# Optimization experiments

Measured on AMD Instinct MI355X. Metric: run time of the kernel, lower is better.

Reference implementation:

```python
import math
import jax, jax.numpy as jnp
import numpy as np

B, L, E, H, NL = 8, 512, 512, 8, 2


def setup_inputs() -> dict:
    key = jax.random.key(0)
    ks = jax.random.split(key, 12)
    s = 0.02  # weight init scale
    return {
        "inputs_4e": jax.random.normal(ks[0], (B, L, 4 * E), jnp.float32),
        "query_embed": jax.random.normal(ks[1], (B, L, E), jnp.float32),
        "rel": jax.random.normal(ks[2], (B, L, L), jnp.float32),
        "resp_rel": jax.random.normal(ks[3], (B, L, L), jnp.float32),
        "timestamp": jax.random.uniform(ks[4], (B, L, L), jnp.float32) * 10.0,
        "l1": jax.random.uniform(ks[5], (1,), jnp.float32),
        "l2": jax.random.uniform(ks[6], (1,), jnp.float32),
        "l3": jax.random.uniform(ks[7], (1,), jnp.float32),
        "Win": jax.random.normal(ks[8], (4 * E, E), jnp.float32) * s,
        "b_in": jnp.zeros((E,), jnp.float32),
        "Wqkv": jax.random.normal(ks[9], (NL, 3, E, E), jnp.float32) * s,
        "bqkv": jnp.zeros((NL, 3, E), jnp.float32),
        "Wf1": jax.random.normal(ks[10], (2 * E, E), jnp.float32) * s,
        "bf1": jnp.zeros((E,), jnp.float32),
        "Wf2": jax.random.normal(ks[11], (E, 1), jnp.float32) * s,
        "bf2": jnp.zeros((1,), jnp.float32),
    }


def _mha(q_in, k_in, v_in, Wq, bq, Wk, bk, Wv, bv,
         rel, resp_rel, timestamp, l1, l2, l3, mask):
    Bb, Ll, Ee = q_in.shape
    d = Ee // H

    def split(x, W, b):  # (B,L,E) -> (B,H,L,d)
        return (x @ W + b).reshape(Bb, Ll, H, d).transpose(0, 2, 1, 3)

    q = split(q_in, Wq, bq)
    k = split(k_in, Wk, bk)
    v = split(v_in, Wv, bv)

    # relation softmax: zero out where mask==False, -1e4 at zeros
    maskf = mask.astype(rel.dtype)              # (1,1,L,L)
    rel_m = rel[:, None, :, :] * maskf          # (B,1,L,L), broadcasts over heads
    rel_attn = jax.nn.softmax(jnp.where(rel_m == 0, -1e4, rel_m), axis=-1)
    resp_m = resp_rel[:, None, :, :] * maskf
    resp_attn = jax.nn.softmax(jnp.where(resp_m == 0, -1e4, resp_m), axis=-1)

    # QK softmax with causal mask
    scores = jnp.einsum('bhqd,bhkd->bhqk', q, k) / math.sqrt(d)
    scores = jnp.where(mask, -1e9, scores)
    prob_attn = jax.nn.softmax(scores, axis=-1)

    # time-decay softmax
    ts = jnp.exp(-jnp.abs(timestamp))[:, None, :, :]  # (B,1,L,L)
    ts = jnp.where(mask, -jnp.inf, ts)
    time_attn = jax.nn.softmax(ts, axis=-1)

    # blend (ablation flags all True)
    p = (1.0 - l2) * prob_attn + l2 * time_attn
    p = (1.0 - l1) * p + l1 * rel_attn
    p = (1.0 - l3) * p + l3 * resp_attn

    out = jnp.einsum('bhqk,bhkd->bhqd', p, v)
    out = out.transpose(0, 2, 1, 3).reshape(Bb, Ll, Ee)
    return out, p


def reference(inputs_4e, query_embed, rel, resp_rel, timestamp,
              l1, l2, l3, Win, b_in, Wqkv, bqkv, Wf1, bf1, Wf2, bf2):
    mask = jnp.triu(jnp.ones((1, 1, L, L), dtype=bool), k=1)  # future mask
    inputs = jax.nn.relu(inputs_4e @ Win + b_in)              # lin_in_interaction

    outputs, attn = _mha(query_embed, inputs, inputs,
                         Wqkv[0, 0], bqkv[0, 0], Wqkv[0, 1], bqkv[0, 1],
                         Wqkv[0, 2], bqkv[0, 2],
                         rel, resp_rel, timestamp, l1, l2, l3, mask)
    for i in range(1, NL):
        residual, attn = _mha(query_embed, outputs, outputs,
                              Wqkv[i, 0], bqkv[i, 0], Wqkv[i, 1], bqkv[i, 1],
                              Wqkv[i, 2], bqkv[i, 2],
                              rel, resp_rel, timestamp, l1, l2, l3, mask)
        outputs = outputs + jax.nn.relu(residual)

    concat_q = jnp.concatenate([outputs, query_embed], axis=-1)  # (B,L,2E)
    h = jax.nn.relu(concat_q @ Wf1 + bf1)
    return h @ Wf2 + bf2  # (B,L,1)
```

## Files before the change

kernel.cpp:

```cpp
#include <hip/hip_runtime.h>
#include <math.h>

namespace {
constexpr int B = 8, L = 512, E = 512, H = 8;
constexpr int M = B * L;
}

typedef float f32x4 __attribute__((ext_vector_type(4)));
typedef short bf16x8 __attribute__((ext_vector_type(8)));

__device__ inline ushort f2b(float f) {
  unsigned u = __float_as_uint(f);
  u += 0x7FFF + ((u >> 16) & 1);
  return (ushort)(u >> 16);
}
__device__ inline float b2f(ushort h) { return __uint_as_float(((unsigned)h) << 16); }

__device__ inline f32x4 mfma16(bf16x8 a, bf16x8 b, f32x4 c) {
  return __builtin_amdgcn_mfma_f32_16x16x32_bf16(a, b, c, 0, 0, 0);
}

__device__ __forceinline__ void gl2lds16(const ushort* g, ushort* l) {
  __builtin_amdgcn_global_load_lds(
      (const __attribute__((address_space(1))) void*)g,
      (__attribute__((address_space(3))) void*)l, 16, 0, 0);
}

template <int NROWS>
__device__ __forceinline__ void stage64(const ushort* __restrict__ g, int ldg,
                                        ushort* lds, int tid) {
  const int w = tid >> 6, l = tid & 63;
  constexpr int RPW = NROWS / 4;
  constexpr int NI = RPW / 8;
#pragma unroll
  for (int it = 0; it < NI; ++it) {
    const int rbase = w * RPW + it * 8;
    const int row = rbase + (l >> 3);
    const int chunk = (l & 7) ^ (row & 7);
    gl2lds16(g + (size_t)row * ldg + chunk * 8, lds + rbase * 64);
  }
}

template <int BM, int NBUF>
__device__ __forceinline__ void stage_comb(const ushort* b0, const ushort* b1,
                                           const ushort* b2, const ushort* b3,
                                           ushort* lds, int tid) {
#pragma unroll
  for (int it = 0; it < BM / 32; ++it) {
    const int row = (tid >> 3) + it * 32;
    const int slot = tid & 7;
    const size_t off = (size_t)row * 512 + slot * 8;
    union Uu { uint4 u; ushort s[8]; } va, vb, vc, vd, vo;
    va.u = *(const uint4*)(b0 + off);
    vb.u = *(const uint4*)(b1 + off);
    if (NBUF == 4) {
      vc.u = *(const uint4*)(b2 + off);
      vd.u = *(const uint4*)(b3 + off);
    }
#pragma unroll
    for (int e = 0; e < 8; ++e) {
      float f = b2f(va.s[e]) + b2f(vb.s[e]);
      if (NBUF == 4) f += fmaxf(b2f(vc.s[e]) + b2f(vd.s[e]), 0.f);
      vo.s[e] = f2b(f);
    }
    *(uint4*)(&lds[row * 64 + ((slot ^ (row & 7)) * 8)]) = vo.u;
  }
}

template <int BM, int MODE, int HAS_BIAS, int ACT, int STAGEA, int FUSE>
__device__ __forceinline__ void dev_gemm(
    ushort* lds, int bxx, int by, const ushort* A, const ushort* A2,
    const ushort* A3, const ushort* A4, const ushort* Aq,
    const ushort* Wt, const float* bias, ushort* C0, ushort* C1, ushort* C2,
    const float* w2, float* outv, int K, int N) {
  ushort* Als = lds;
  ushort* Bls = lds + 2 * BM * 64;
  const int tid = threadIdx.x;
  const int l = tid & 63, wv = tid >> 6;
  const int wr = wv >> 1, wc = wv & 1;
  const int g = l >> 4, c = l & 15;
  constexpr int WM = BM / 2;
  constexpr int MFR = WM / 16;
  const int bm = by * BM;
  const int bn64 = bxx * 64;
  const int sec = (MODE == 5) ? (bn64 >> 9) : 0;
  const bool vsec = (MODE == 5 && sec == 1);

  const ushort* Ause = (MODE == 5) ? A2 : A;
  const int ldA = K;
  const ushort* Bp = Wt + (size_t)bn64 * K;

  f32x4 acc[MFR][2];
#pragma unroll
  for (int mi = 0; mi < MFR; ++mi)
#pragma unroll
    for (int ni = 0; ni < 2; ++ni) acc[mi][ni] = f32x4{0.f, 0.f, 0.f, 0.f};

  auto stageA = [&](int t, int buf) {
    ushort* dst = Als + buf * BM * 64;
    if (STAGEA == 0) {
      stage64<BM>(Ause + (size_t)bm * ldA + t * 64, ldA, dst, tid);
    } else if (STAGEA == 2) {
      stage_comb<BM, 2>(A + (size_t)bm * 512 + t * 64,
                        A2 + (size_t)bm * 512 + t * 64, nullptr, nullptr, dst, tid);
    } else {
      if (t < 8)
        stage_comb<BM, 4>(A + (size_t)bm * 512 + t * 64,
                          A2 + (size_t)bm * 512 + t * 64,
                          A3 + (size_t)bm * 512 + t * 64,
                          A4 + (size_t)bm * 512 + t * 64, dst, tid);
      else
        stage64<BM>(Aq + (size_t)bm * 512 + (t - 8) * 64, 512, dst, tid);
    }
  };

  stageA(0, 0);
  stage64<64>(Bp, K, Bls, tid);
  __syncthreads();

  const int NT = K >> 6;
  int cur = 0;
  for (int t = 0; t < NT; ++t) {
    if (t + 1 < NT) {
      stageA(t + 1, cur ^ 1);
      stage64<64>(Bp + (t + 1) * 64, K, Bls + (cur ^ 1) * 64 * 64, tid);
    }
#pragma unroll
    for (int ks = 0; ks < 2; ++ks) {
      bf16x8 af[MFR], bf_[2];
#pragma unroll
      for (int mi = 0; mi < MFR; ++mi) {
        const int row = wr * WM + mi * 16 + c;
        af[mi] = *(const bf16x8*)(&Als[cur * BM * 64 + row * 64 +
                                       (((ks * 4 + g) ^ (row & 7)) * 8)]);
      }
#pragma unroll
      for (int ni = 0; ni < 2; ++ni) {
        const int row = wc * 32 + ni * 16 + c;
        bf_[ni] = *(const bf16x8*)(&Bls[cur * 64 * 64 + row * 64 +
                                        (((ks * 4 + g) ^ (row & 7)) * 8)]);
      }
      if (vsec) {
#pragma unroll
        for (int mi = 0; mi < MFR; ++mi)
#pragma unroll
          for (int ni = 0; ni < 2; ++ni)
            acc[mi][ni] = mfma16(bf_[ni], af[mi], acc[mi][ni]);
      } else {
#pragma unroll
        for (int mi = 0; mi < MFR; ++mi)
#pragma unroll
          for (int ni = 0; ni < 2; ++ni)
            acc[mi][ni] = mfma16(af[mi], bf_[ni], acc[mi][ni]);
      }
    }
    __syncthreads();
    cur ^= 1;
  }

  if (FUSE) {
    float w2v[2];
#pragma unroll
    for (int ni = 0; ni < 2; ++ni) w2v[ni] = w2[bn64 + wc * 32 + ni * 16 + c];
#pragma unroll
    for (int mi = 0; mi < MFR; ++mi) {
#pragma unroll
      for (int r = 0; r < 4; ++r) {
        float p = 0.f;
#pragma unroll
        for (int ni = 0; ni < 2; ++ni) {
          const int n = bn64 + wc * 32 + ni * 16 + c;
          float v = acc[mi][ni][r] + bias[n];
          v = fmaxf(v, 0.f);
          p += v * w2v[ni];
        }
        p += __shfl_xor(p, 1);
        p += __shfl_xor(p, 2);
        p += __shfl_xor(p, 4);
        p += __shfl_xor(p, 8);
        if (c == 0) atomicAdd(&outv[bm + wr * WM + mi * 16 + g * 4 + r], p);
      }
    }
  } else if (vsec) {
    const int e0 = bn64 - 512;
#pragma unroll
    for (int ni = 0; ni < 2; ++ni) {
#pragma unroll
      for (int r = 0; r < 4; ++r) {
        const int e = e0 + wc * 32 + ni * 16 + g * 4 + r;
        const float bv = HAS_BIAS ? bias[512 + e] : 0.f;
#pragma unroll
        for (int mi = 0; mi < MFR; ++mi) {
          const int m = bm + wr * WM + mi * 16 + c;
          const int bb = m >> 9, lt = m & 511;
          C2[((size_t)bb * 512 + e) * 512 + lt] = f2b(acc[mi][ni][r] + bv);
        }
      }
    }
  } else {
    ushort* dst = (MODE == 5) ? C1 : C0;
    const int nsub = (MODE == 5) ? sec * 512 : 0;
    const int ldc = (MODE == 5) ? 512 : N;
#pragma unroll
    for (int ni = 0; ni < 2; ++ni) {
      const int n = bn64 + wc * 32 + ni * 16 + c;
      const float bv = HAS_BIAS ? bias[n] : 0.f;
#pragma unroll
      for (int mi = 0; mi < MFR; ++mi) {
#pragma unroll
        for (int r = 0; r < 4; ++r) {
          const int m = bm + wr * WM + mi * 16 + g * 4 + r;
          float v = acc[mi][ni][r] + bv;
          if (ACT) v = fmaxf(v, 0.f);
          dst[(size_t)m * ldc + (n - nsub)] = f2b(v);
        }
      }
    }
  }
}

__device__ __forceinline__ void dev_attn(ushort* lds, int qt, int h, int b,
                                         const ushort* __restrict__ Qg,
                                         const ushort* __restrict__ Kg,
                                         const ushort* __restrict__ Vt,
                                         float c_p, ushort* __restrict__ aexp) {
  ushort* Qs = lds;
  ushort* Ps = lds + 4096;
  ushort* Ks = lds + 8192;
  ushort* Vs = lds + 16384;
  const int tid = threadIdx.x, l = tid & 63, w = tid >> 6;
  const int g = l >> 4, c = l & 15;
  const int qrow0 = b * L + qt * 64;
  const ushort* Kbase = Kg + (size_t)(b * L) * E + h * 64;
  const ushort* Vbase = Vt + (size_t)(b * E + h * 64) * L;

  stage64<64>(Qg + (size_t)qrow0 * E + h * 64, E, Qs, tid);
  stage64<64>(Kbase, E, Ks, tid);
  stage64<64>(Vbase, L, Vs, tid);
  __syncthreads();

  f32x4 o[4];
#pragma unroll
  for (int dn = 0; dn < 4; ++dn) o[dn] = f32x4{0.f, 0.f, 0.f, 0.f};
  float l_r[4] = {0.f, 0.f, 0.f, 0.f};

  int cur = 0;
  for (int kt = 0; kt <= qt; ++kt) {
    if (kt < qt) {
      stage64<64>(Kbase + (size_t)(kt + 1) * 64 * E, E, Ks + (cur ^ 1) * 4096, tid);
      stage64<64>(Vbase + (kt + 1) * 64, L, Vs + (cur ^ 1) * 4096, tid);
    }
    bf16x8 qf[2];
#pragma unroll
    for (int kq = 0; kq < 2; ++kq) {
      int row = w * 16 + c;
      qf[kq] = *(const bf16x8*)(&Qs[row * 64 + (((kq * 4 + g) ^ (row & 7)) * 8)]);
    }
    f32x4 s4[4];
#pragma unroll
    for (int n = 0; n < 4; ++n) s4[n] = f32x4{0.f, 0.f, 0.f, 0.f};
#pragma unroll
    for (int n = 0; n < 4; ++n) {
#pragma unroll
      for (int kq = 0; kq < 2; ++kq) {
        int row = n * 16 + c;
        bf16x8 kf = *(const bf16x8*)(&Ks[cur * 4096 + row * 64 +
                                         (((kq * 4 + g) ^ (row & 7)) * 8)]);
        s4[n] = mfma16(qf[kq], kf, s4[n]);
      }
    }
    const bool diag = (kt == qt);
    float pv[4][4];
    float lad[4] = {0.f, 0.f, 0.f, 0.f};
#pragma unroll
    for (int n = 0; n < 4; ++n)
#pragma unroll
      for (int r = 0; r < 4; ++r) {
        float sv = s4[n][r] * 0.125f;
        if (diag && (n * 16 + c) > (w * 16 + g * 4 + r)) sv = -1e30f;
        float p = __expf(sv);
        pv[n][r] = p;
        lad[r] += p;
      }
#pragma unroll
    for (int off = 1; off < 16; off <<= 1)
#pragma unroll
      for (int r = 0; r < 4; ++r) lad[r] += __shfl_xor(lad[r], off);
#pragma unroll
    for (int r = 0; r < 4; ++r) l_r[r] += lad[r];
#pragma unroll
    for (int n = 0; n < 4; ++n)
#pragma unroll
      for (int r = 0; r < 4; ++r) {
        int q = w * 16 + g * 4 + r;
        int byt = 32 * n + 2 * c;
        int slot = byt >> 4;
        Ps[q * 64 + ((slot ^ (q & 7)) * 8) + ((byt & 15) >> 1)] = f2b(pv[n][r]);
      }
    bf16x8 pf[2];
#pragma unroll
    for (int kq = 0; kq < 2; ++kq) {
      int row = w * 16 + c;
      pf[kq] = *(const bf16x8*)(&Ps[row * 64 + (((kq * 4 + g) ^ (row & 7)) * 8)]);
    }
#pragma unroll
    for (int dn = 0; dn < 4; ++dn) {
#pragma unroll
      for (int kq = 0; kq < 2; ++kq) {
        int row = dn * 16 + c;
        bf16x8 vf = *(const bf16x8*)(&Vs[cur * 4096 + row * 64 +
                                         (((kq * 4 + g) ^ (row & 7)) * 8)]);
        o[dn] = mfma16(pf[kq], vf, o[dn]);
      }
    }
    __syncthreads();
    cur ^= 1;
  }

  float linv[4];
#pragma unroll
  for (int r = 0; r < 4; ++r) linv[r] = c_p / l_r[r];
#pragma unroll
  for (int dn = 0; dn < 4; ++dn) {
#pragma unroll
    for (int r = 0; r < 4; ++r) {
      const size_t row = (size_t)qrow0 + w * 16 + g * 4 + r;
      const int col = h * 64 + dn * 16 + c;
      aexp[row * E + col] = f2b(o[dn][r] * linv[r]);
    }
  }
}

__device__ __forceinline__ void dev_blend(int idx, const float* __restrict__ rel,
                                          const float* __restrict__ resp,
                                          const float* __restrict__ ts,
                                          float l1, float l2, float l3,
                                          ushort* __restrict__ stat) {
  const float c_t = (1.f - l3) * (1.f - l1) * l2;
  const float c_r = (1.f - l3) * l1;
  const float c_s = l3;
  const int wave = threadIdx.x >> 6, lane = threadIdx.x & 63;
  const int row = idx * 4 + wave;
  const int qi = row & (L - 1);
  const size_t base = (size_t)row * L;
  float rv[8], sv[8], tv[8];
#pragma unroll
  for (int jj = 0; jj < 8; ++jj) {
    const int k = jj * 64 + lane;
    const float r = rel[base + k];
    const float s = resp[base + k];
    const float tt = ts[base + k];
    const bool fut = (k > qi);
    const float rm = fut ? r : 0.f;
    const float sm = fut ? s : 0.f;
    rv[jj] = (rm == 0.f) ? -1e4f : rm;
    sv[jj] = (sm == 0.f) ? -1e4f : sm;
    tv[jj] = fut ? -INFINITY : __expf(-fabsf(tt));
  }
  float rmax = -INFINITY, smax = -INFINITY, tmax = -INFINITY;
#pragma unroll
  for (int jj = 0; jj < 8; ++jj) {
    rmax = fmaxf(rmax, rv[jj]); smax = fmaxf(smax, sv[jj]); tmax = fmaxf(tmax, tv[jj]);
  }
  for (int off = 1; off < 64; off <<= 1) {
    rmax = fmaxf(rmax, __shfl_xor(rmax, off));
    smax = fmaxf(smax, __shfl_xor(smax, off));
    tmax = fmaxf(tmax, __shfl_xor(tmax, off));
  }
  float rsum = 0.f, ssum = 0.f, tsum = 0.f;
#pragma unroll
  for (int jj = 0; jj < 8; ++jj) {
    rsum += __expf(rv[jj] - rmax); ssum += __expf(sv[jj] - smax); tsum += __expf(tv[jj] - tmax);
  }
  for (int off = 1; off < 64; off <<= 1) {
    rsum += __shfl_xor(rsum, off);
    ssum += __shfl_xor(ssum, off);
    tsum += __shfl_xor(tsum, off);
  }
  const float rinv = c_r / rsum, sinv = c_s / ssum, tinv = c_t / tsum;
#pragma unroll
  for (int jj = 0; jj < 8; ++jj) {
    stat[base + jj * 64 + lane] =
        f2b(__expf(rv[jj] - rmax) * rinv + __expf(sv[jj] - smax) * sinv +
            __expf(tv[jj] - tmax) * tinv);
  }
}

__device__ __forceinline__ void tcvt_body(const float* __restrict__ src,
                                          ushort* __restrict__ dst, int Kd, int Nd,
                                          int kb, int nb, int t, ushort (*T)[33]) {
  const int r = t >> 3, c4 = (t & 7) * 4;
  float4 v = *(const float4*)(src + (size_t)(kb + r) * Nd + nb + c4);
  T[r][c4 + 0] = f2b(v.x); T[r][c4 + 1] = f2b(v.y);
  T[r][c4 + 2] = f2b(v.z); T[r][c4 + 3] = f2b(v.w);
  __syncthreads();
  ushort4 ov = {T[c4 + 0][r], T[c4 + 1][r], T[c4 + 2][r], T[c4 + 3][r]};
  *(ushort4*)(&dst[(size_t)(nb + r) * Kd + kb + c4]) = ov;
}

__global__ __launch_bounds__(256) void k_prep(
    const float* __restrict__ x4e, const float* __restrict__ query,
    const float* __restrict__ Win, const float* __restrict__ Wqkv,
    const float* __restrict__ bf2, ushort* __restrict__ x4e_bf,
    ushort* __restrict__ qbf, ushort* __restrict__ Wint,
    ushort* __restrict__ Wqkvt, float* __restrict__ outv) {
  __shared__ ushort T[32][33];
  const int bi = blockIdx.x;
  const int t = threadIdx.x;
  const long long EE = (long long)E * E;
  if (bi < 2560) {
    const int N1 = M * 2048 / 4;
#pragma unroll
    for (int it = 0; it < 4; ++it) {
      int i = bi * 1024 + it * 256 + t;
      if (i < N1) {
        float4 v = ((const float4*)x4e)[i];
        ushort4 o = {f2b(v.x), f2b(v.y), f2b(v.z), f2b(v.w)};
        ((ushort4*)x4e_bf)[i] = o;
      } else {
        int j = i - N1;
        float4 v = ((const float4*)query)[j];
        ushort4 o = {f2b(v.x), f2b(v.y), f2b(v.z), f2b(v.w)};
        ((ushort4*)qbf)[j] = o;
      }
    }
    return;
  }
  if (bi < 3584) {
    const int idx = bi - 2560;
    tcvt_body(Win, Wint, 2048, 512, (idx >> 4) * 32, (idx & 15) * 32, t, T);
    return;
  }
  if (bi < 4096) {
    const int idx = bi - 3584;
    const int z = (idx >= 256) ? 3 : 0;
    const int r = idx & 255;
    tcvt_body(Wqkv + z * EE, Wqkvt + z * EE, 512, 512, (r >> 4) * 32,
              (r & 15) * 32, t, T);
    return;
  }
  {
    const int i = (bi - 4096) * 256 + t;
    const float b2 = bf2[0];
    float4 v = {b2, b2, b2, b2};
    ((float4*)outv)[i] = v;
  }
}

__global__ __launch_bounds__(256) void k_xgemm_blend(
    const ushort* __restrict__ x4e_bf, const ushort* __restrict__ query_bf,
    const ushort* __restrict__ Wint, const ushort* __restrict__ Wqkvt,
    const float* __restrict__ b_in, const float* __restrict__ bqkv,
    ushort* __restrict__ x_bf, ushort* __restrict__ q_bf,
    ushort* __restrict__ q1_bf, const float* __restrict__ Wqkv,
    const float* __restrict__ Wf1, ushort* __restrict__ Wqkvt_out,
    ushort* __restrict__ Wf1t, const float* __restrict__ rel,
    const float* __restrict__ resp, const float* __restrict__ ts,
    const float* __restrict__ l1p, const float* __restrict__ l2p,
    const float* __restrict__ l3p, ushort* __restrict__ stat) {
  extern __shared__ ushort lds[];
  const int bx = blockIdx.x;
  const long long EE = (long long)E * E;
  if (bx < 256) {
    dev_gemm<128, 1, 1, 1, 0, 0>(lds, bx >> 5, bx & 31, x4e_bf, nullptr, nullptr,
                                 nullptr, nullptr, Wint, b_in, x_bf, nullptr,
                                 nullptr, nullptr, nullptr, 2048, 512);
  } else if (bx < 512) {
    const int r = bx - 256;
    dev_gemm<128, 1, 1, 0, 0, 0>(lds, r >> 5, r & 31, query_bf, nullptr, nullptr,
                                 nullptr, nullptr, Wqkvt, bqkv, q_bf, nullptr,
                                 nullptr, nullptr, nullptr, 512, 512);
  } else if (bx < 768) {
    const int r = bx - 512;
    dev_gemm<128, 1, 1, 0, 0, 0>(lds, r >> 5, r & 31, query_bf, nullptr, nullptr,
                                 nullptr, nullptr, Wqkvt + 3 * EE, bqkv + 3 * E,
                                 q1_bf, nullptr, nullptr, nullptr, nullptr, 512, 512);
  } else if (bx < 1792) {
    const int idx = bx - 768;
    const int zmap[4] = {1, 2, 4, 5};
    const int z = zmap[idx >> 8];
    const int r = idx & 255;
    tcvt_body(Wqkv + z * EE, Wqkvt_out + z * EE, 512, 512, (r >> 4) * 32,
              (r & 15) * 32, threadIdx.x, (ushort(*)[33])lds);
  } else if (bx < 2304) {
    const int q = bx - 1792;
    tcvt_body(Wf1, Wf1t, 1024, 512, (q >> 4) * 32, (q & 15) * 32,
              threadIdx.x, (ushort(*)[33])lds);
  } else {
    dev_blend(bx - 2304, rel, resp, ts, l1p[0], l2p[0], l3p[0], stat);
  }
}

__global__ __launch_bounds__(256) void k_kv0(
    const ushort* __restrict__ x_bf, const ushort* __restrict__ Wt,
    const float* __restrict__ bias, ushort* __restrict__ k_bf,
    ushort* __restrict__ vt) {
  extern __shared__ ushort lds[];
  const int bx = blockIdx.x;
  dev_gemm<128, 5, 1, 0, 0, 0>(lds, bx >> 5, bx & 31, nullptr, x_bf,
                               nullptr, nullptr, nullptr, Wt, bias, nullptr,
                               k_bf, vt, nullptr, nullptr, 512, 1024);
}

__global__ __launch_bounds__(256) void k_attn_stat(
    const ushort* __restrict__ Qg, const ushort* __restrict__ Kg,
    const ushort* __restrict__ Vt, const ushort* __restrict__ stat,
    const float* __restrict__ l1p, const float* __restrict__ l2p,
    const float* __restrict__ l3p, ushort* __restrict__ aexp,
    ushort* __restrict__ ostat) {
  extern __shared__ ushort lds[];
  const int bx = blockIdx.x;
  if (bx < 512) {
    const int hb = bx & 63;
    const int qt = 7 - (bx >> 6);
    const int h = hb & 7, b = hb >> 3;
    const float l1 = l1p[0], l2 = l2p[0], l3 = l3p[0];
    const float c_p = (1.f - l3) * (1.f - l1) * (1.f - l2);
    dev_attn(lds, qt, h, b, Qg, Kg, Vt, c_p, aexp);
  } else {
    const int idx = bx - 512;
    const int n = idx >> 5;
    const int rem = idx & 31;
    const int bz = rem >> 2, m = rem & 3;
    const long long LLs = (long long)L * L, ELs = (long long)E * L;
    dev_gemm<128, 1, 0, 0, 0, 0>(lds, n, m, stat + bz * LLs, nullptr,
                                 nullptr, nullptr, nullptr, Vt + bz * ELs,
                                 nullptr, ostat + bz * ELs, nullptr, nullptr,
                                 nullptr, nullptr, 512, 512);
  }
}

__global__ __launch_bounds__(256) void k_kv1(
    const ushort* __restrict__ aexp0, const ushort* __restrict__ ostat0,
    const ushort* __restrict__ Wt, const float* __restrict__ bias,
    ushort* __restrict__ k_bf, ushort* __restrict__ vt) {
  extern __shared__ ushort lds[];
  const int bx = blockIdx.x;
  dev_gemm<128, 5, 1, 0, 2, 0>(lds, bx >> 5, bx & 31, aexp0, ostat0,
                               nullptr, nullptr, nullptr, Wt, bias, nullptr,
                               k_bf, vt, nullptr, nullptr, 512, 1024);
}

__global__ __launch_bounds__(256) void k_f1(
    const ushort* __restrict__ aexp0, const ushort* __restrict__ ostat0,
    const ushort* __restrict__ aexp1, const ushort* __restrict__ ostat1,
    const ushort* __restrict__ query_bf, const ushort* __restrict__ Wf1t,
    const float* __restrict__ bf1, const float* __restrict__ Wf2,
    float* __restrict__ outv) {
  extern __shared__ ushort lds[];
  const int bx = blockIdx.x;
  dev_gemm<128, 4, 1, 1, 4, 1>(lds, bx >> 5, bx & 31, aexp0, ostat0,
                               aexp1, ostat1, query_bf, Wf1t, bf1, nullptr,
                               nullptr, nullptr, Wf2, outv, 1024, 512);
}

extern "C" void kernel_launch(void* const* d_in, const int* in_sizes, int n_in,
                              void* d_out, int out_size, void* d_ws, size_t ws_size,
                              hipStream_t stream) {
  (void)in_sizes; (void)n_in; (void)out_size; (void)ws_size;
  const float* inputs_4e = (const float*)d_in[0];
  const float* query = (const float*)d_in[1];
  const float* rel = (const float*)d_in[2];
  const float* resp = (const float*)d_in[3];
  const float* tsp = (const float*)d_in[4];
  const float* l1p = (const float*)d_in[5];
  const float* l2p = (const float*)d_in[6];
  const float* l3p = (const float*)d_in[7];
  const float* Win = (const float*)d_in[8];
  const float* b_in = (const float*)d_in[9];
  const float* Wqkv = (const float*)d_in[10];
  const float* bqkv = (const float*)d_in[11];
  const float* Wf1 = (const float*)d_in[12];
  const float* bf1 = (const float*)d_in[13];
  const float* Wf2 = (const float*)d_in[14];
  const float* bf2 = (const float*)d_in[15];

  char* ws = (char*)d_ws;
  const size_t MB = 1ull << 20;
  ushort* x4e_bf  = (ushort*)(ws + 0 * MB);
  ushort* aexp0   = (ushort*)(ws + 0 * MB);
  ushort* ostat0  = (ushort*)(ws + 4 * MB);
  ushort* aexp1   = (ushort*)(ws + 8 * MB);
  ushort* ostat1  = (ushort*)(ws + 12 * MB);
  ushort* query_bf= (ushort*)(ws + 16 * MB);
  ushort* stat_bf = (ushort*)(ws + 20 * MB);
  ushort* x_bf    = (ushort*)(ws + 24 * MB);
  ushort* q_bf    = (ushort*)(ws + 28 * MB);
  ushort* k_bf    = (ushort*)(ws + 32 * MB);
  ushort* vt      = (ushort*)(ws + 36 * MB);
  ushort* q1_bf   = (ushort*)(ws + 40 * MB);
  ushort* Wint    = (ushort*)(ws + 48 * MB);
  ushort* Wqkvt   = (ushort*)(ws + 50 * MB);
  ushort* Wf1t    = (ushort*)(ws + 53 * MB);

  const long long EE = (long long)E * E;
  const int LDS_G128 = (2 * 128 * 64 + 2 * 64 * 64) * 2;
  const int LDS_AS = 49152;

  k_prep<<<2560 + 1024 + 512 + 4, 256, 0, stream>>>(
      inputs_4e, query, Win, Wqkv, bf2, x4e_bf, query_bf, Wint, Wqkvt,
      (float*)d_out);
  k_xgemm_blend<<<256 + 512 + 1024 + 512 + 1024, 256, LDS_G128, stream>>>(
      x4e_bf, query_bf, Wint, Wqkvt, b_in, bqkv, x_bf, q_bf, q1_bf,
      Wqkv, Wf1, Wqkvt, Wf1t, rel, resp, tsp, l1p, l2p, l3p, stat_bf);
  k_kv0<<<512, 256, LDS_G128, stream>>>(x_bf, Wqkvt + 1 * EE,
                                        bqkv + 1 * E, k_bf, vt);
  k_attn_stat<<<768, 256, LDS_AS, stream>>>(q_bf, k_bf, vt, stat_bf,
                                            l1p, l2p, l3p, aexp0, ostat0);
  k_kv1<<<512, 256, LDS_G128, stream>>>(aexp0, ostat0, Wqkvt + 4 * EE,
                                        bqkv + 4 * E, k_bf, vt);
  k_attn_stat<<<768, 256, LDS_AS, stream>>>(q1_bf, k_bf, vt, stat_bf,
                                            l1p, l2p, l3p, aexp1, ostat1);
  k_f1<<<256, 256, LDS_G128, stream>>>(aexp0, ostat0, aexp1, ostat1,
                                       query_bf, Wf1t, bf1, Wf2,
                                       (float*)d_out);
}
```

Baseline: 119.9 us.

## Rebalance independent work across stage kernels, overlapping blend with KV GEMM

Moves the relation/time blend and the layer-1 and Wf1 weight transposes out of the first GEMM kernel into the KV0 GEMM kernel. Stage two now runs only the input and query GEMMs plus the layer-0 K/V weight transposes that KV0 needs. The aim is to balance block counts so independent memory-bound work fills the GPU alongside the compute-bound KV GEMM. It risks contention between GEMM and bandwidth-heavy blend blocks, and it relies on the dependency ordering staying correct.

```diff
diff --git a/kernel.cpp b/kernel.cpp
--- a/kernel.cpp
+++ b/kernel.cpp
@@ -447,17 +447,13 @@
   }
 }
 
-__global__ __launch_bounds__(256) void k_xgemm_blend(
+__global__ __launch_bounds__(256) void k_stage2(
     const ushort* __restrict__ x4e_bf, const ushort* __restrict__ query_bf,
     const ushort* __restrict__ Wint, const ushort* __restrict__ Wqkvt,
     const float* __restrict__ b_in, const float* __restrict__ bqkv,
     ushort* __restrict__ x_bf, ushort* __restrict__ q_bf,
     ushort* __restrict__ q1_bf, const float* __restrict__ Wqkv,
-    const float* __restrict__ Wf1, ushort* __restrict__ Wqkvt_out,
-    ushort* __restrict__ Wf1t, const float* __restrict__ rel,
-    const float* __restrict__ resp, const float* __restrict__ ts,
-    const float* __restrict__ l1p, const float* __restrict__ l2p,
-    const float* __restrict__ l3p, ushort* __restrict__ stat) {
+    ushort* __restrict__ Wqkvt_out) {
   extern __shared__ ushort lds[];
   const int bx = blockIdx.x;
   const long long EE = (long long)E * E;
@@ -475,31 +471,44 @@
     dev_gemm<128, 1, 1, 0, 0, 0>(lds, r >> 5, r & 31, query_bf, nullptr, nullptr,
                                  nullptr, nullptr, Wqkvt + 3 * EE, bqkv + 3 * E,
                                  q1_bf, nullptr, nullptr, nullptr, nullptr, 512, 512);
-  } else if (bx < 1792) {
+  } else {
     const int idx = bx - 768;
-    const int zmap[4] = {1, 2, 4, 5};
-    const int z = zmap[idx >> 8];
+    const int z = 1 + (idx >> 8);
     const int r = idx & 255;
     tcvt_body(Wqkv + z * EE, Wqkvt_out + z * EE, 512, 512, (r >> 4) * 32,
               (r & 15) * 32, threadIdx.x, (ushort(*)[33])lds);
-  } else if (bx < 2304) {
-    const int q = bx - 1792;
+  }
+}
+
+__global__ __launch_bounds__(256) void k_stage3(
+    const ushort* __restrict__ x_bf, const ushort* __restrict__ Wt,
+    const float* __restrict__ bias, ushort* __restrict__ k_bf,
+    ushort* __restrict__ vt, const float* __restrict__ rel,
+    const float* __restrict__ resp, const float* __restrict__ ts,
+    const float* __restrict__ l1p, const float* __restrict__ l2p,
+    const float* __restrict__ l3p, ushort* __restrict__ stat,
+    const float* __restrict__ Wqkv, ushort* __restrict__ Wqkvt_out,
+    const float* __restrict__ Wf1, ushort* __restrict__ Wf1t) {
+  extern __shared__ ushort lds[];
+  const int bx = blockIdx.x;
+  const long long EE = (long long)E * E;
+  if (bx < 512) {
+    dev_gemm<128, 5, 1, 0, 0, 0>(lds, bx >> 5, bx & 31, nullptr, x_bf,
+                                 nullptr, nullptr, nullptr, Wt, bias, nullptr,
+                                 k_bf, vt, nullptr, nullptr, 512, 1024);
+  } else if (bx < 1536) {
+    dev_blend(bx - 512, rel, resp, ts, l1p[0], l2p[0], l3p[0], stat);
+  } else if (bx < 2048) {
+    const int idx = bx - 1536;
+    const int z = 4 + (idx >> 8);
+    const int r = idx & 255;
+    tcvt_body(Wqkv + z * EE, Wqkvt_out + z * EE, 512, 512, (r >> 4) * 32,
+              (r & 15) * 32, threadIdx.x, (ushort(*)[33])lds);
+  } else {
+    const int q = bx - 2048;
     tcvt_body(Wf1, Wf1t, 1024, 512, (q >> 4) * 32, (q & 15) * 32,
               threadIdx.x, (ushort(*)[33])lds);
-  } else {
-    dev_blend(bx - 2304, rel, resp, ts, l1p[0], l2p[0], l3p[0], stat);
-  }
-}
-
-__global__ __launch_bounds__(256) void k_kv0(
-    const ushort* __restrict__ x_bf, const ushort* __restrict__ Wt,
-    const float* __restrict__ bias, ushort* __restrict__ k_bf,
-    ushort* __restrict__ vt) {
-  extern __shared__ ushort lds[];
-  const int bx = blockIdx.x;
-  dev_gemm<128, 5, 1, 0, 0, 0>(lds, bx >> 5, bx & 31, nullptr, x_bf,
-                               nullptr, nullptr, nullptr, Wt, bias, nullptr,
-                               k_bf, vt, nullptr, nullptr, 512, 1024);
+  }
 }
 
 __global__ __launch_bounds__(256) void k_attn_stat(
@@ -600,11 +609,12 @@
   k_prep<<<2560 + 1024 + 512 + 4, 256, 0, stream>>>(
       inputs_4e, query, Win, Wqkv, bf2, x4e_bf, query_bf, Wint, Wqkvt,
       (float*)d_out);
-  k_xgemm_blend<<<256 + 512 + 1024 + 512 + 1024, 256, LDS_G128, stream>>>(
+  k_stage2<<<256 + 256 + 256 + 512, 256, LDS_G128, stream>>>(
       x4e_bf, query_bf, Wint, Wqkvt, b_in, bqkv, x_bf, q_bf, q1_bf,
-      Wqkv, Wf1, Wqkvt, Wf1t, rel, resp, tsp, l1p, l2p, l3p, stat_bf);
-  k_kv0<<<512, 256, LDS_G128, stream>>>(x_bf, Wqkvt + 1 * EE,
-                                        bqkv + 1 * E, k_bf, vt);
+      Wqkv, Wqkvt);
+  k_stage3<<<512 + 1024 + 512 + 512, 256, LDS_G128, stream>>>(
+      x_bf, Wqkvt + 1 * EE, bqkv + 1 * E, k_bf, vt,
+      rel, resp, tsp, l1p, l2p, l3p, stat_bf, Wqkv, Wqkvt, Wf1, Wf1t);
   k_attn_stat<<<768, 256, LDS_AS, stream>>>(q_bf, k_bf, vt, stat_bf,
                                             l1p, l2p, l3p, aexp0, ostat0);
   k_kv1<<<512, 256, LDS_G128, stream>>>(aexp0, ostat0, Wqkvt + 4 * EE,
```

Result: slower. 125.9 us (+5.0%).
